# Kernel optimization log

Hardware: AMD Instinct MI355X
Metric: run time of the kernel (lower is better)

The kernel has to match this reference:

```python
import jax, jax.numpy as jnp
import numpy as np

B, M, D, O = 64, 4096, 128, 16


def setup_inputs() -> dict:
    key = jax.random.key(0)
    k1, k2, k3, k4 = jax.random.split(key, 4)
    glorot_w = float(np.sqrt(6.0 / (D + D)))
    glorot_v = float(np.sqrt(6.0 / (2 * D + 1)))
    return {
        "x1": jax.random.normal(k1, (B, D), dtype=jnp.float32),
        "x2": jax.random.normal(k2, (B, M, D), dtype=jnp.float32),
        "W": jax.random.uniform(k3, (O, D, D), minval=-glorot_w, maxval=glorot_w, dtype=jnp.float32),
        "V": jax.random.uniform(k4, (O, 2 * D, 1), minval=-glorot_v, maxval=glorot_v, dtype=jnp.float32),
        "bias": jnp.zeros((O,), dtype=jnp.float32),
    }


def reference(x1, x2, W, V, bias):
    d = x1.shape[1]
    # Bilinear term: x1 . W[o] . x2^T for every output slice o -> [B, M, O]
    s1 = jnp.einsum('bd,odk,bmk->bmo', x1, W, x2)
    # Linear term: V[o]^T concat(x1_tiled, x2). Split V into the x1 part and x2 part.
    v1 = V[:, :d, 0]   # [O, D]
    v2 = V[:, d:, 0]   # [O, D]
    s2 = jnp.einsum('bd,od->bo', x1, v1)[:, None, :] + jnp.einsum('bmd,od->bmo', x2, v2)
    out = jax.nn.relu(s1 + s2 + bias)  # [B, M, O]
    return out.reshape(-1, out.shape[-1])  # [B*M, O], matches concat of [-1,1] slices
```

## Files before the change

### kernel.cpp

```cpp
#include <hip/hip_runtime.h>

#define B_ 64
#define M_ 4096
#define D_ 128
#define O_ 16

typedef __bf16 bf16x8 __attribute__((ext_vector_type(8)));
typedef float  f32x4  __attribute__((ext_vector_type(4)));

__global__ __launch_bounds__(128) void prep_kernel(
    const float* __restrict__ x1, const float* __restrict__ W,
    const float* __restrict__ V, const float* __restrict__ bias,
    __bf16* __restrict__ ub, float* __restrict__ c)
{
    const int o = blockIdx.x;
    const int b = blockIdx.y;
    const int k = threadIdx.x;
    __shared__ float x1s[D_];
    __shared__ float red[2];
    x1s[k] = x1[b * D_ + k];
    __syncthreads();

    const float* Wo = W + o * D_ * D_;
    float acc = 0.f;
    #pragma unroll 8
    for (int d = 0; d < D_; ++d)
        acc = fmaf(x1s[d], Wo[d * D_ + k], acc);

    const float uval = acc + V[o * 2 * D_ + D_ + k];
    const int e  = k & 7;
    const int g  = (k >> 3) & 3;
    const int kb = k >> 5;
    ub[(size_t)b * 2048 + kb * 512 + g * 128 + o * 8 + e] = (__bf16)uval;

    float p = x1s[k] * V[o * 2 * D_ + k];
    #pragma unroll
    for (int off = 32; off; off >>= 1) p += __shfl_down(p, off, 64);
    if ((k & 63) == 0) red[k >> 6] = p;
    __syncthreads();
    if (k == 0) c[b * O_ + o] = red[0] + red[1] + bias[o];
}

__global__ __launch_bounds__(256, 8) void fused_kernel(
    const float* __restrict__ x2, const __bf16* __restrict__ ub,
    const float* __restrict__ c, float* __restrict__ out)
{
    const int b = blockIdx.y;
    const int t = threadIdx.x;
    const int wave = t >> 6, lane = t & 63;
    const int rc = lane & 15;
    const int g  = lane >> 4;

    const bf16x8* uf = (const bf16x8*)(ub + (size_t)b * 2048);
    bf16x8 bfrag[4];
    #pragma unroll
    for (int kb = 0; kb < 4; ++kb) bfrag[kb] = uf[kb * 64 + lane];
    const float cv = c[b * O_ + rc];

    const int m_base = blockIdx.x * 128 + wave * 32;

    #pragma unroll
    for (int tt = 0; tt < 2; ++tt) {
        const int m0 = m_base + tt * 16;
        const float4* ap = (const float4*)(x2 + ((size_t)b * M_ + m0 + rc) * D_) + g * 2;

        float4 c0 = ap[0], c1 = ap[1];
        f32x4 acc = {cv, cv, cv, cv};
        #pragma unroll
        for (int kb = 0; kb < 4; ++kb) {
            float4 n0, n1;
            if (kb < 3) { n0 = ap[(kb + 1) * 8]; n1 = ap[(kb + 1) * 8 + 1]; }
            bf16x8 af;
            af[0] = (__bf16)c0.x; af[1] = (__bf16)c0.y;
            af[2] = (__bf16)c0.z; af[3] = (__bf16)c0.w;
            af[4] = (__bf16)c1.x; af[5] = (__bf16)c1.y;
            af[6] = (__bf16)c1.z; af[7] = (__bf16)c1.w;
            acc = __builtin_amdgcn_mfma_f32_16x16x32_bf16(af, bfrag[kb], acc, 0, 0, 0);
            c0 = n0; c1 = n1;
        }

        float* op = out + ((size_t)b * M_ + m0) * O_ + rc;
        #pragma unroll
        for (int i = 0; i < 4; ++i)
            op[(g * 4 + i) * O_] = fmaxf(acc[i], 0.f);
    }
}

extern "C" void kernel_launch(void* const* d_in, const int* in_sizes, int n_in,
                              void* d_out, int out_size, void* d_ws, size_t ws_size,
                              hipStream_t stream) {
    const float* x1   = (const float*)d_in[0];
    const float* x2   = (const float*)d_in[1];
    const float* W    = (const float*)d_in[2];
    const float* V    = (const float*)d_in[3];
    const float* bias = (const float*)d_in[4];
    float* out = (float*)d_out;

    __bf16* ubf = (__bf16*)d_ws;
    float*  c   = (float*)((char*)d_ws + (size_t)B_ * 2048 * sizeof(__bf16));

    prep_kernel<<<dim3(O_, B_), 128, 0, stream>>>(x1, W, V, bias, ubf, c);
    fused_kernel<<<dim3(M_ / 128, B_), 256, 0, stream>>>(x2, ubf, c, out);
}
```

Before: 35.10 us.

## Fuse prep and main kernels with per-batch atomic flag synchronisation

Merges the prep and MFMA kernels into one launch. Each of the 32 blocks for a batch computes a 64-wide slice of u = x1·W[o]+v2, then bumps a per-batch atomic counter. Every block spins until all 32 producers for its batch are done, computes the x1·v1+bias term locally, and stores output with nontemporal stores. This removes the second launch and the gap between kernels, but adds a memset launch, spin-waiting that depends on all producer blocks being co-resident (deadlock risk), and repeated work for the c term.

```diff
diff --git a/kernel.cpp b/kernel.cpp
--- a/kernel.cpp
+++ b/kernel.cpp
@@ -8,56 +8,71 @@
 typedef __bf16 bf16x8 __attribute__((ext_vector_type(8)));
 typedef float  f32x4  __attribute__((ext_vector_type(4)));
 
-__global__ __launch_bounds__(128) void prep_kernel(
-    const float* __restrict__ x1, const float* __restrict__ W,
-    const float* __restrict__ V, const float* __restrict__ bias,
-    __bf16* __restrict__ ub, float* __restrict__ c)
+__global__ __launch_bounds__(256, 6) void ntn_kernel(
+    const float* __restrict__ x1, const float* __restrict__ x2,
+    const float* __restrict__ W,  const float* __restrict__ V,
+    const float* __restrict__ bias,
+    __bf16* __restrict__ ub, int* __restrict__ flags,
+    float* __restrict__ out)
 {
-    const int o = blockIdx.x;
-    const int b = blockIdx.y;
-    const int k = threadIdx.x;
+    const int bid   = blockIdx.x;
+    const int b     = bid >> 5;
+    const int chunk = bid & 31;
+    const int t     = threadIdx.x;
+
     __shared__ float x1s[D_];
-    __shared__ float red[2];
-    x1s[k] = x1[b * D_ + k];
+    if (t < D_) x1s[t] = x1[b * D_ + t];
     __syncthreads();
 
-    const float* Wo = W + o * D_ * D_;
-    float acc = 0.f;
-    #pragma unroll 8
-    for (int d = 0; d < D_; ++d)
-        acc = fmaf(x1s[d], Wo[d * D_ + k], acc);
+    {
+        const int o     = chunk >> 1;
+        const int kbase = (chunk & 1) * 64;
+        const int j     = t >> 2;
+        const int q     = t & 3;
+        const int k     = kbase + j;
+        const float* Wp = W + ((size_t)o * D_ + q * 32) * D_ + k;
+        float p = 0.f;
+        #pragma unroll 8
+        for (int dd = 0; dd < 32; ++dd)
+            p = fmaf(x1s[q * 32 + dd], Wp[(size_t)dd * D_], p);
+        p += __shfl_xor(p, 1, 64);
+        p += __shfl_xor(p, 2, 64);
+        if (q == 0) {
+            const float uval = p + V[o * 2 * D_ + D_ + k];
+            const int e  = k & 7;
+            const int g  = (k >> 3) & 3;
+            const int kb = k >> 5;
+            ub[(size_t)b * 2048 + kb * 512 + g * 128 + o * 8 + e] = (__bf16)uval;
+        }
+        __syncthreads();
+        if (t == 0) {
+            __threadfence();
+            atomicAdd(&flags[b], 1);
+        }
+    }
 
-    const float uval = acc + V[o * 2 * D_ + D_ + k];
-    const int e  = k & 7;
-    const int g  = (k >> 3) & 3;
-    const int kb = k >> 5;
-    ub[(size_t)b * 2048 + kb * 512 + g * 128 + o * 8 + e] = (__bf16)uval;
-
-    float p = x1s[k] * V[o * 2 * D_ + k];
-    #pragma unroll
-    for (int off = 32; off; off >>= 1) p += __shfl_down(p, off, 64);
-    if ((k & 63) == 0) red[k >> 6] = p;
-    __syncthreads();
-    if (k == 0) c[b * O_ + o] = red[0] + red[1] + bias[o];
-}
-
-__global__ __launch_bounds__(256, 8) void fused_kernel(
-    const float* __restrict__ x2, const __bf16* __restrict__ ub,
-    const float* __restrict__ c, float* __restrict__ out)
-{
-    const int b = blockIdx.y;
-    const int t = threadIdx.x;
     const int wave = t >> 6, lane = t & 63;
     const int rc = lane & 15;
     const int g  = lane >> 4;
+
+    float cv = bias[rc];
+    #pragma unroll 8
+    for (int k = 0; k < D_; ++k)
+        cv = fmaf(x1s[k], V[rc * 2 * D_ + k], cv);
+
+    if (t == 0) {
+        while (__hip_atomic_load(&flags[b], __ATOMIC_ACQUIRE,
+                                 __HIP_MEMORY_SCOPE_AGENT) < 32)
+            __builtin_amdgcn_s_sleep(1);
+    }
+    __syncthreads();
 
     const bf16x8* uf = (const bf16x8*)(ub + (size_t)b * 2048);
     bf16x8 bfrag[4];
     #pragma unroll
     for (int kb = 0; kb < 4; ++kb) bfrag[kb] = uf[kb * 64 + lane];
-    const float cv = c[b * O_ + rc];
 
-    const int m_base = blockIdx.x * 128 + wave * 32;
+    const int m_base = chunk * 128 + wave * 32;
 
     #pragma unroll
     for (int tt = 0; tt < 2; ++tt) {
@@ -82,7 +97,7 @@
         float* op = out + ((size_t)b * M_ + m0) * O_ + rc;
         #pragma unroll
         for (int i = 0; i < 4; ++i)
-            op[(g * 4 + i) * O_] = fmaxf(acc[i], 0.f);
+            __builtin_nontemporal_store(fmaxf(acc[i], 0.f), &op[(g * 4 + i) * O_]);
     }
 }
 
@@ -96,9 +111,10 @@
     const float* bias = (const float*)d_in[4];
     float* out = (float*)d_out;
 
-    __bf16* ubf = (__bf16*)d_ws;
-    float*  c   = (float*)((char*)d_ws + (size_t)B_ * 2048 * sizeof(__bf16));
+    __bf16* ubf  = (__bf16*)d_ws;
+    int*    flgs = (int*)((char*)d_ws + (size_t)B_ * 2048 * sizeof(__bf16));
 
-    prep_kernel<<<dim3(O_, B_), 128, 0, stream>>>(x1, W, V, bias, ubf, c);
-    fused_kernel<<<dim3(M_ / 128, B_), 256, 0, stream>>>(x2, ubf, c, out);
+    hipMemsetAsync(flgs, 0, B_ * sizeof(int), stream);
+    ntn_kernel<<<dim3(B_ * 32), 256, 0, stream>>>(x1, x2, W, V, bias,
+                                                  ubf, flgs, out);
 }
```

Result: slower. 119.1 us (+239.4%).
